# Kernel optimization log

Hardware: AMD Instinct MI355X
Metric: run time of the kernel (lower is better)

Reference implementation:

```python
import jax, jax.numpy as jnp
import numpy as np

EPS = 1e-8  # torch.cosine_similarity eps


def setup_inputs() -> dict:
    key = jax.random.key(0)
    ks = jax.random.split(key, 6)
    B, D, R, T = 131072, 512, 128, 3
    return {
        "x_encoded": jax.random.normal(ks[0], (B, D), dtype=jnp.float32),
        "register": jax.random.normal(ks[1], (R, D), dtype=jnp.float32),
        "W": jax.random.normal(ks[2], (D, D), dtype=jnp.float32) / np.sqrt(D),
        "b": jax.random.normal(ks[3], (D,), dtype=jnp.float32) * 0.01,
        "low_rank_u": jax.random.normal(ks[4], (T,), dtype=jnp.float32),
        "low_rank_v": jax.random.normal(ks[5], (D,), dtype=jnp.float32),
        "k": 3,
    }


def reference(x_encoded, register, W, b, low_rank_u, low_rank_v, k):
    # mode='finetune' path of TSRegister.get_register_tokens
    # data_projection: Linear(d_model, d_model)
    xe = x_encoded @ W.T + b                      # [B, D]
    # cosine similarity vs codebook: dot / max(|x||r|, eps)
    xn = jnp.linalg.norm(xe, axis=-1)             # [B]
    rn = jnp.linalg.norm(register, axis=-1)       # [R]
    sims = (xe @ register.T) / jnp.maximum(xn[:, None] * rn[None, :], EPS)  # [B, R]
    top_k_values, top_k_indices = jax.lax.top_k(sims, k)  # [B, k]
    selected_centers = register[top_k_indices]    # gather -> [B, k, D]
    adaptation_matrix = jnp.outer(low_rank_u, low_rank_v)  # [k, D] (k == num_register_tokens)
    adapted_centers = selected_centers + adaptation_matrix[None, :, :]
    return adapted_centers, top_k_indices, top_k_values
```

## Files before the change

kernel.cpp:

```cpp
#include <hip/hip_runtime.h>
#include <hip/hip_bf16.h>

#define TSTR 68
#define SSTR 129

__global__ void rn_kernel(const float* __restrict__ cb, float* __restrict__ rn) {
    const int j = blockIdx.x;
    const int t = threadIdx.x;
    double a = 0.0;
#pragma unroll
    for (int m = 0; m < 8; ++m) {
        float f = cb[j * 512 + m * 64 + t];
        a += (double)f * (double)f;
    }
#pragma unroll
    for (int off = 32; off >= 1; off >>= 1)
        a += __shfl_down(a, off);
    if (t == 0) rn[j] = (float)sqrt(a);
}

__global__ __launch_bounds__(256, 2) void fused_kernel(
    const float* __restrict__ x, const float* __restrict__ cb,
    const float* __restrict__ W, const float* __restrict__ bias,
    const float* __restrict__ u, const float* __restrict__ v,
    const float* __restrict__ rn, float* __restrict__ out,
    size_t idx_off, size_t val_off)
{
    __shared__ __align__(16) float uA[128 * TSTR];
    __shared__ __align__(16) float xeL[64 * TSTR];
    __shared__ float rnL[128];
    __shared__ int   idxL[64 * 3];

    const int tid = threadIdx.x;
    const int tlo = tid & 15;
    const int thi = tid >> 4;
    const int row0 = blockIdx.x << 6;

    if (tid < 128) rnL[tid] = rn[tid];

    const int srow = tid >> 2;
    const int scol = (tid & 3) << 4;

    float m2[4][8];
#pragma unroll
    for (int i = 0; i < 4; ++i)
#pragma unroll
        for (int j = 0; j < 8; ++j) m2[i][j] = 0.f;
    float nacc = 0.f;

    for (int dc = 0; dc < 8; ++dc) {
        float m1[4][4];
#pragma unroll
        for (int i = 0; i < 4; ++i)
#pragma unroll
            for (int j = 0; j < 4; ++j) m1[i][j] = 0.f;

        for (int kc = 0; kc < 8; ++kc) {
            __syncthreads();
            {
                const float4* gx = (const float4*)(x + (size_t)(row0 + srow) * 512 + kc * 64 + scol);
                const float4* gw = (const float4*)(W + (size_t)(dc * 64 + srow) * 512 + kc * 64 + scol);
                float4* dx = (float4*)&uA[srow * TSTR + scol];
                float4* dw = (float4*)&uA[64 * TSTR + srow * TSTR + scol];
#pragma unroll
                for (int m = 0; m < 4; ++m) { dx[m] = gx[m]; dw[m] = gw[m]; }
            }
            __syncthreads();
            float s1[4][4];
#pragma unroll
            for (int i = 0; i < 4; ++i)
#pragma unroll
                for (int j = 0; j < 4; ++j) s1[i][j] = 0.f;
#pragma unroll
            for (int kk = 0; kk < 16; ++kk) {
                float4 xa[4], wa[4];
#pragma unroll
                for (int i = 0; i < 4; ++i)
                    xa[i] = *(const float4*)&uA[(thi + 16 * i) * TSTR + (kk << 2)];
#pragma unroll
                for (int j = 0; j < 4; ++j)
                    wa[j] = *(const float4*)&uA[64 * TSTR + (tlo + 16 * j) * TSTR + (kk << 2)];
#pragma unroll
                for (int i = 0; i < 4; ++i)
#pragma unroll
                    for (int j = 0; j < 4; ++j) {
                        s1[i][j] = fmaf(xa[i].x, wa[j].x, s1[i][j]);
                        s1[i][j] = fmaf(xa[i].y, wa[j].y, s1[i][j]);
                        s1[i][j] = fmaf(xa[i].z, wa[j].z, s1[i][j]);
                        s1[i][j] = fmaf(xa[i].w, wa[j].w, s1[i][j]);
                    }
            }
#pragma unroll
            for (int i = 0; i < 4; ++i)
#pragma unroll
                for (int j = 0; j < 4; ++j) m1[i][j] += s1[i][j];
        }
#pragma unroll
        for (int j = 0; j < 4; ++j) {
            float bj = bias[dc * 64 + tlo + 16 * j];
#pragma unroll
            for (int i = 0; i < 4; ++i)
                xeL[(thi + 16 * i) * TSTR + tlo + 16 * j] = m1[i][j] + bj;
        }
        __syncthreads();
        {
            const float4* gr = (const float4*)(cb + (size_t)(tid >> 1) * 512 + dc * 64 + ((tid & 1) << 5));
            float4* dr = (float4*)&uA[(tid >> 1) * TSTR + ((tid & 1) << 5)];
#pragma unroll
            for (int m = 0; m < 8; ++m) dr[m] = gr[m];
        }
        if (tid < 64) {
#pragma unroll
            for (int dd = 0; dd < 16; ++dd) {
                float4 q = *(const float4*)&xeL[tid * TSTR + (dd << 2)];
                nacc = fmaf(q.x, q.x, nacc);
                nacc = fmaf(q.y, q.y, nacc);
                nacc = fmaf(q.z, q.z, nacc);
                nacc = fmaf(q.w, q.w, nacc);
            }
        }
        __syncthreads();
        float s2[4][8];
#pragma unroll
        for (int i = 0; i < 4; ++i)
#pragma unroll
            for (int j = 0; j < 8; ++j) s2[i][j] = 0.f;
#pragma unroll
        for (int dd = 0; dd < 16; ++dd) {
            float4 xv[4], rv[8];
#pragma unroll
            for (int i = 0; i < 4; ++i)
                xv[i] = *(const float4*)&xeL[(tlo + 16 * i) * TSTR + (dd << 2)];
#pragma unroll
            for (int j = 0; j < 8; ++j)
                rv[j] = *(const float4*)&uA[(thi + 16 * j) * TSTR + (dd << 2)];
#pragma unroll
            for (int i = 0; i < 4; ++i)
#pragma unroll
                for (int j = 0; j < 8; ++j) {
                    s2[i][j] = fmaf(xv[i].x, rv[j].x, s2[i][j]);
                    s2[i][j] = fmaf(xv[i].y, rv[j].y, s2[i][j]);
                    s2[i][j] = fmaf(xv[i].z, rv[j].z, s2[i][j]);
                    s2[i][j] = fmaf(xv[i].w, rv[j].w, s2[i][j]);
                }
        }
#pragma unroll
        for (int i = 0; i < 4; ++i)
#pragma unroll
            for (int j = 0; j < 8; ++j) m2[i][j] += s2[i][j];
    }
    __syncthreads();
#pragma unroll
    for (int i = 0; i < 4; ++i)
#pragma unroll
        for (int j = 0; j < 8; ++j)
            uA[(tlo + 16 * i) * SSTR + thi + 16 * j] = m2[i][j];
    __syncthreads();

    if (tid < 64) {
        float xn = sqrtf(nacc);
        float b0 = -1e30f, b1 = -1e30f, b2 = -1e30f;
        int i0 = 0, i1 = 0, i2 = 0;
        for (int j = 0; j < 128; ++j) {
            float s = uA[tid * SSTR + j] / fmaxf(xn * rnL[j], 1e-8f);
            if (s > b0)      { b2 = b1; i2 = i1; b1 = b0; i1 = i0; b0 = s; i0 = j; }
            else if (s > b1) { b2 = b1; i2 = i1; b1 = s;  i1 = j; }
            else if (s > b2) { b2 = s;  i2 = j; }
        }
        const size_t g = (size_t)(row0 + tid);
        float* oi = out + idx_off + g * 3;
        oi[0] = (float)i0;
        oi[1] = (float)i1;
        oi[2] = (float)i2;
        float* ov = out + val_off + g * 3;
        ov[0] = b0;
        ov[1] = b1;
        ov[2] = b2;
        idxL[tid * 3 + 0] = i0; idxL[tid * 3 + 1] = i1; idxL[tid * 3 + 2] = i2;
    }
    __syncthreads();

    {
        const int arow = tid >> 2;
        const int seg  = tid & 3;
#pragma unroll
        for (int tt = 0; tt < 3; ++tt) {
            const int idx = idxL[arow * 3 + tt];
            const float uu = u[tt];
            const float4* gr4 = (const float4*)(cb + (size_t)idx * 512 + seg * 128);
            const float4* gv4 = (const float4*)(v + seg * 128);
            float4* ob = (float4*)(out + ((size_t)(row0 + arow) * 3 + tt) * 512 + seg * 128);
#pragma unroll
            for (int c = 0; c < 32; ++c) {
                float4 rv = gr4[c];
                float4 vv = gv4[c];
                float4 o;
                o.x = fmaf(uu, vv.x, rv.x);
                o.y = fmaf(uu, vv.y, rv.y);
                o.z = fmaf(uu, vv.z, rv.z);
                o.w = fmaf(uu, vv.w, rv.w);
                ob[c] = o;
            }
        }
    }
}

extern "C" void kernel_launch(void* const* d_in, const int* in_sizes, int n_in,
                              void* d_out, int out_size, void* d_ws, size_t ws_size,
                              hipStream_t stream) {
    const float* x  = (const float*)d_in[0];
    const float* cb = (const float*)d_in[1];
    const float* W  = (const float*)d_in[2];
    const float* b  = (const float*)d_in[3];
    const float* u  = (const float*)d_in[4];
    const float* v  = (const float*)d_in[5];
    float* rn = (float*)d_ws;
    float* out = (float*)d_out;

    const size_t B = (size_t)in_sizes[0] / 512;
    const size_t val_off = (size_t)out_size - 3 * B;
    const size_t idx_off = (size_t)out_size - 6 * B;

    hipLaunchKernelGGL(rn_kernel, dim3(128), dim3(64), 0, stream, cb, rn);
    hipLaunchKernelGGL(fused_kernel, dim3((unsigned)(B / 64)), dim3(256), 0, stream,
                       x, cb, W, b, u, v, rn, out, idx_off, val_off);
}
```

Baseline: 1.737 ms.

## Parallelize top-3 selection across four lanes per row with packed keys

Replaces the serial per-row top-3 scan, which ran on only 64 threads, with a 4-lanes-per-row scan. Each lane packs score and column into a sortable 64-bit key, and the lanes merge via xor shuffles. The gather/adapt output phase is remapped to 12 tasks per row. Launch bounds are raised to 3 blocks per CU to increase occupancy, which risks register spills in the GEMM accumulators.

```diff
diff --git a/kernel.cpp b/kernel.cpp
--- a/kernel.cpp
+++ b/kernel.cpp
@@ -1,8 +1,28 @@
 #include <hip/hip_runtime.h>
-#include <hip/hip_bf16.h>
 
 #define TSTR 68
+#define XESTR 68
 #define SSTR 129
+
+__device__ __forceinline__ unsigned long long pack_key(float s, int col) {
+    unsigned u = __float_as_uint(s);
+    unsigned m = (u & 0x80000000u) ? ~u : (u | 0x80000000u);
+    return ((unsigned long long)m << 32) | (unsigned)(127 - col);
+}
+__device__ __forceinline__ float key_val(unsigned long long k) {
+    unsigned m = (unsigned)(k >> 32);
+    unsigned u = (m & 0x80000000u) ? (m ^ 0x80000000u) : ~m;
+    return __uint_as_float(u);
+}
+__device__ __forceinline__ int key_col(unsigned long long k) {
+    return 127 - (int)(k & 0xFFFFFFFFu);
+}
+__device__ __forceinline__ void ins3(unsigned long long x,
+        unsigned long long &a0, unsigned long long &a1, unsigned long long &a2) {
+    if (x > a0)      { a2 = a1; a1 = a0; a0 = x; }
+    else if (x > a1) { a2 = a1; a1 = x; }
+    else if (x > a2) { a2 = x; }
+}
 
 __global__ void rn_kernel(const float* __restrict__ cb, float* __restrict__ rn) {
     const int j = blockIdx.x;
@@ -19,7 +39,7 @@
     if (t == 0) rn[j] = (float)sqrt(a);
 }
 
-__global__ __launch_bounds__(256, 2) void fused_kernel(
+__global__ __launch_bounds__(256, 3) void fused_kernel(
     const float* __restrict__ x, const float* __restrict__ cb,
     const float* __restrict__ W, const float* __restrict__ bias,
     const float* __restrict__ u, const float* __restrict__ v,
@@ -27,9 +47,10 @@
     size_t idx_off, size_t val_off)
 {
     __shared__ __align__(16) float uA[128 * TSTR];
-    __shared__ __align__(16) float xeL[64 * TSTR];
+    __shared__ __align__(16) float xeL[64 * XESTR];
     __shared__ float rnL[128];
-    __shared__ int   idxL[64 * 3];
+    __shared__ float xnL[64];
+    __shared__ unsigned char idxL[64 * 3];
 
     const int tid = threadIdx.x;
     const int tlo = tid & 15;
@@ -100,7 +121,7 @@
             float bj = bias[dc * 64 + tlo + 16 * j];
 #pragma unroll
             for (int i = 0; i < 4; ++i)
-                xeL[(thi + 16 * i) * TSTR + tlo + 16 * j] = m1[i][j] + bj;
+                xeL[(thi + 16 * i) * XESTR + tlo + 16 * j] = m1[i][j] + bj;
         }
         __syncthreads();
         {
@@ -112,7 +133,7 @@
         if (tid < 64) {
 #pragma unroll
             for (int dd = 0; dd < 16; ++dd) {
-                float4 q = *(const float4*)&xeL[tid * TSTR + (dd << 2)];
+                float4 q = *(const float4*)&xeL[tid * XESTR + (dd << 2)];
                 nacc = fmaf(q.x, q.x, nacc);
                 nacc = fmaf(q.y, q.y, nacc);
                 nacc = fmaf(q.z, q.z, nacc);
@@ -130,7 +151,7 @@
             float4 xv[4], rv[8];
 #pragma unroll
             for (int i = 0; i < 4; ++i)
-                xv[i] = *(const float4*)&xeL[(tlo + 16 * i) * TSTR + (dd << 2)];
+                xv[i] = *(const float4*)&xeL[(tlo + 16 * i) * XESTR + (dd << 2)];
 #pragma unroll
             for (int j = 0; j < 8; ++j)
                 rv[j] = *(const float4*)&uA[(thi + 16 * j) * TSTR + (dd << 2)];
@@ -155,52 +176,63 @@
 #pragma unroll
         for (int j = 0; j < 8; ++j)
             uA[(tlo + 16 * i) * SSTR + thi + 16 * j] = m2[i][j];
+    if (tid < 64) xnL[tid] = sqrtf(nacc);
     __syncthreads();
 
-    if (tid < 64) {
-        float xn = sqrtf(nacc);
-        float b0 = -1e30f, b1 = -1e30f, b2 = -1e30f;
-        int i0 = 0, i1 = 0, i2 = 0;
-        for (int j = 0; j < 128; ++j) {
-            float s = uA[tid * SSTR + j] / fmaxf(xn * rnL[j], 1e-8f);
-            if (s > b0)      { b2 = b1; i2 = i1; b1 = b0; i1 = i0; b0 = s; i0 = j; }
-            else if (s > b1) { b2 = b1; i2 = i1; b1 = s;  i1 = j; }
-            else if (s > b2) { b2 = s;  i2 = j; }
-        }
-        const size_t g = (size_t)(row0 + tid);
-        float* oi = out + idx_off + g * 3;
-        oi[0] = (float)i0;
-        oi[1] = (float)i1;
-        oi[2] = (float)i2;
-        float* ov = out + val_off + g * 3;
-        ov[0] = b0;
-        ov[1] = b1;
-        ov[2] = b2;
-        idxL[tid * 3 + 0] = i0; idxL[tid * 3 + 1] = i1; idxL[tid * 3 + 2] = i2;
+    {
+        const int row = tid >> 2;
+        const int p   = tid & 3;
+        const float xn = xnL[row];
+        unsigned long long a0 = 0, a1 = 0, a2 = 0;
+#pragma unroll
+        for (int t = 0; t < 32; ++t) {
+            const int c = p + 4 * t;
+            float s = uA[row * SSTR + c] / fmaxf(xn * rnL[c], 1e-8f);
+            ins3(pack_key(s, c), a0, a1, a2);
+        }
+#pragma unroll
+        for (int mask = 1; mask <= 2; mask <<= 1) {
+            unsigned long long b0 = __shfl_xor(a0, mask);
+            unsigned long long b1 = __shfl_xor(a1, mask);
+            unsigned long long b2 = __shfl_xor(a2, mask);
+            ins3(b0, a0, a1, a2); ins3(b1, a0, a1, a2); ins3(b2, a0, a1, a2);
+        }
+        if (p == 0) {
+            const size_t g = (size_t)(row0 + row);
+            float* oi = out + idx_off + g * 3;
+            float* ov = out + val_off + g * 3;
+            oi[0] = (float)key_col(a0); oi[1] = (float)key_col(a1); oi[2] = (float)key_col(a2);
+            ov[0] = key_val(a0); ov[1] = key_val(a1); ov[2] = key_val(a2);
+            idxL[row * 3 + 0] = (unsigned char)key_col(a0);
+            idxL[row * 3 + 1] = (unsigned char)key_col(a1);
+            idxL[row * 3 + 2] = (unsigned char)key_col(a2);
+        }
     }
     __syncthreads();
 
-    {
-        const int arow = tid >> 2;
-        const int seg  = tid & 3;
-#pragma unroll
-        for (int tt = 0; tt < 3; ++tt) {
-            const int idx = idxL[arow * 3 + tt];
-            const float uu = u[tt];
-            const float4* gr4 = (const float4*)(cb + (size_t)idx * 512 + seg * 128);
-            const float4* gv4 = (const float4*)(v + seg * 128);
-            float4* ob = (float4*)(out + ((size_t)(row0 + arow) * 3 + tt) * 512 + seg * 128);
-#pragma unroll
-            for (int c = 0; c < 32; ++c) {
-                float4 rv = gr4[c];
-                float4 vv = gv4[c];
-                float4 o;
-                o.x = fmaf(uu, vv.x, rv.x);
-                o.y = fmaf(uu, vv.y, rv.y);
-                o.z = fmaf(uu, vv.z, rv.z);
-                o.w = fmaf(uu, vv.w, rv.w);
-                ob[c] = o;
-            }
+    const float uu0 = u[0], uu1 = u[1], uu2 = u[2];
+#pragma unroll
+    for (int q = 0; q < 3; ++q) {
+        int task = tid + 256 * q;
+        int row = task / 12;
+        int rem = task - row * 12;
+        int tt  = rem >> 2;
+        int seg = rem & 3;
+        int idx = idxL[row * 3 + tt];
+        float uu = (tt == 0) ? uu0 : ((tt == 1) ? uu1 : uu2);
+        const float4* gr4 = (const float4*)(cb + (size_t)idx * 512 + seg * 128);
+        const float4* gv4 = (const float4*)(v + seg * 128);
+        float4* ob = (float4*)(out + ((size_t)(row0 + row) * 3 + tt) * 512 + seg * 128);
+#pragma unroll
+        for (int c2 = 0; c2 < 32; ++c2) {
+            float4 rv = gr4[c2];
+            float4 vv = gv4[c2];
+            float4 o;
+            o.x = fmaf(uu, vv.x, rv.x);
+            o.y = fmaf(uu, vv.y, rv.y);
+            o.z = fmaf(uu, vv.z, rv.z);
+            o.w = fmaf(uu, vv.w, rv.w);
+            ob[c2] = o;
         }
     }
 }
```

Result: faster. 1.644 ms (-5.4%).
